# Optimization experiments

Hardware: AMD Instinct MI355X
Metric: run time of the kernel (lower is better)

The kernel has to match this reference:

```python
import jax, jax.numpy as jnp
import numpy as np

# Shapes / hyperparams (match init_kwargs and input_specs)
B, CIN, COUT, H, W = 8, 128, 128, 64, 64
K, S, P, D = 3, 1, 1, 1
KK = K * K
EPS = 1e-5  # BatchNorm eps


def setup_inputs() -> dict:
    key = jax.random.key(0)
    ks = jax.random.split(key, 4)
    x = jax.random.normal(ks[0], (B, CIN, H, W), jnp.float32)
    # small offset weights so predicted offsets stay O(1) pixels
    w_off = jax.random.normal(ks[1], (2 * KK, CIN, K, K), jnp.float32) * 0.01
    w_def = jax.random.normal(ks[2], (COUT, CIN, K, K), jnp.float32) * (1.0 / np.sqrt(CIN * KK))
    b_def = jax.random.normal(ks[3], (COUT,), jnp.float32) * 0.01
    gamma = jnp.ones((COUT,), jnp.float32)
    beta = jnp.zeros((COUT,), jnp.float32)
    return dict(x=x, w_off=w_off, w_def=w_def, b_def=b_def, gamma=gamma, beta=beta)


def _bilinear_gather(x, ys, xs):
    """x: [B,C,H,W]; ys/xs: [B,KK,Ho,Wo] float coords -> [B,C,KK,Ho,Wo].
    Zero padding outside the image (torchvision DeformConv2d semantics)."""
    Bb, C, Hh, Ww = x.shape
    y0 = jnp.floor(ys)
    x0 = jnp.floor(xs)
    wy = ys - y0
    wx = xs - x0
    xf = x.reshape(Bb, C, Hh * Ww)

    def gather(yi, xi, w):
        valid = (yi >= 0) & (yi < Hh) & (xi >= 0) & (xi < Ww)
        idx = (jnp.clip(yi, 0, Hh - 1) * Ww + jnp.clip(xi, 0, Ww - 1)).astype(jnp.int32)
        g = jnp.take_along_axis(xf, idx.reshape(Bb, 1, -1), axis=2)  # [B,C,KK*Ho*Wo]
        g = g.reshape(Bb, C, *idx.shape[1:])  # [B,C,KK,Ho,Wo]
        return g * (w * valid)[:, None]

    return (gather(y0, x0, (1 - wy) * (1 - wx))
            + gather(y0, x0 + 1, (1 - wy) * wx)
            + gather(y0 + 1, x0, wy * (1 - wx))
            + gather(y0 + 1, x0 + 1, wy * wx))


def _forward(x, w_off, w_def, b_def, gamma, beta):
    # 1) offset prediction: standard conv, no bias
    offset = jax.lax.conv_general_dilated(
        x, w_off, window_strides=(S, S), padding=((P, P), (P, P)),
        rhs_dilation=(D, D), dimension_numbers=('NCHW', 'OIHW', 'NCHW'))
    Ho, Wo = offset.shape[2], offset.shape[3]
    off = offset.reshape(B, KK, 2, Ho, Wo)  # (dy, dx) pairs per kernel loc
    dy, dx = off[:, :, 0], off[:, :, 1]

    # 2) deformable sampling coordinates
    ky = (jnp.arange(KK) // K).astype(jnp.float32) * D  # kernel row offset
    kx = (jnp.arange(KK) % K).astype(jnp.float32) * D   # kernel col offset
    base_y = (jnp.arange(Ho) * S - P).astype(jnp.float32)
    base_x = (jnp.arange(Wo) * S - P).astype(jnp.float32)
    ys = base_y[None, None, :, None] + ky[None, :, None, None] + dy  # [B,KK,Ho,Wo]
    xs = base_x[None, None, None, :] + kx[None, :, None, None] + dx

    sampled = _bilinear_gather(x, ys, xs)  # [B,CIN,KK,Ho,Wo]

    # 3) per-kernel-location weighted accumulation (implicit GEMM) + bias
    out = jnp.einsum('bckhw,ock->bohw', sampled, w_def.reshape(COUT, CIN, KK))
    out = out + b_def[None, :, None, None]

    # 4) BatchNorm2d (training mode: batch statistics) + SiLU
    mean = out.mean(axis=(0, 2, 3))
    var = out.var(axis=(0, 2, 3))
    scale = gamma / jnp.sqrt(var + EPS)
    out = (out - mean[None, :, None, None]) * scale[None, :, None, None] + beta[None, :, None, None]
    return out * jax.nn.sigmoid(out)  # SiLU


def reference(x, w_off, w_def, b_def, gamma, beta):
    return _forward(x, w_off, w_def, b_def, gamma, beta)
```

## Files before the change

### kernel.cpp

```cpp
#include <hip/hip_runtime.h>
#include <math.h>

#define CIN   128
#define COUT  128
#define KKT   9
#define NSTAT 32768.0f

typedef __attribute__((ext_vector_type(8))) short bf16x8;
typedef __attribute__((ext_vector_type(4))) float f32x4;
typedef __attribute__((ext_vector_type(2))) float f32x2;

__device__ inline unsigned short f2bf(float f) {
    union { float f; unsigned u; } v; v.f = f;
    unsigned r = v.u + 0x7fffu + ((v.u >> 16) & 1u);
    return (unsigned short)(r >> 16);
}
__device__ inline f32x2 bf2(unsigned u) {
    union { unsigned u; float f; } lo, hi;
    lo.u = u << 16; hi.u = u & 0xffff0000u;
    f32x2 r; r[0] = lo.f; r[1] = hi.f; return r;
}

#define PUB_BARRIER() do { asm volatile("s_waitcnt lgkmcnt(0)" ::: "memory"); \
                           __builtin_amdgcn_s_barrier(); } while (0)


__global__ __launch_bounds__(512) void prep_all_k(const float* __restrict__ x,
                                                  unsigned* __restrict__ xt,
                                                  const float* __restrict__ w_def,
                                                  const float* __restrict__ w_off,
                                                  unsigned short* __restrict__ wb,
                                                  unsigned short* __restrict__ wob,
                                                  float* __restrict__ sums) {
    __shared__ float lt[128][65];
    const int bb = blockIdx.x;
    if (bb < 512) {
        const int b = bb >> 6, y = bb & 63;
        const int t = threadIdx.x, l = t & 63, g8 = t >> 6;
        const float* xb = x + (b * 128) * 4096 + y * 64;
#pragma unroll
        for (int pass = 0; pass < 16; pass++) {
            int c = pass * 8 + g8;
            lt[c][l] = xb[c * 4096 + l];
        }
        __syncthreads();
        unsigned* xo = xt + (bb * 64) * 64;
#pragma unroll
        for (int pass = 0; pass < 8; pass++) {
            int w = pass * 8 + g8;
            float f0 = lt[2 * l][w], f1 = lt[2 * l + 1][w];
            xo[w * 64 + l] = (unsigned)f2bf(f0) | ((unsigned)f2bf(f1) << 16);
        }
    } else {
        int i = (bb - 512) * 512 + threadIdx.x;
        if (i < 147456) {
            int oc = i / 1152, r = i - oc * 1152, kt = r >> 7, c = r & 127;
            wb[i] = f2bf(w_def[(oc * 128 + c) * 9 + kt]);
        } else if (i < 147456 + 36864) {
            int j = i - 147456;
            int ocp = j / 1152, r = j - ocp * 1152, kt = r >> 7, c = r & 127;
            wob[j] = (ocp < 18) ? f2bf(w_off[(ocp * 128 + c) * 9 + kt]) : (unsigned short)0;
        } else if (i < 147456 + 36864 + 256) {
            sums[i - 147456 - 36864] = 0.f;
        }
    }
}

__global__ __launch_bounds__(1024, 8) void deform_main_k(const unsigned* __restrict__ xt,
                                                         const unsigned short* __restrict__ wb,
                                                         const unsigned short* __restrict__ wob,
                                                         const float* __restrict__ b_def,
                                                         float* __restrict__ out,
                                                         float* __restrict__ sums,
                                                         float* __restrict__ sumsq) {
    __shared__ __align__(16) unsigned char smem[52224];
    unsigned short* xrow  = (unsigned short*)smem;
    int*            tab   = (int*)smem;
    unsigned short* samp0 = (unsigned short*)(smem + 18432);
    unsigned short* samp1 = (unsigned short*)(smem + 34816);
    float* offl = (float*)(smem + 34816);
    float* stat = (float*)(smem + 51200);

    const int t    = threadIdx.x;
    const int bh   = blockIdx.x;
    const int b    = bh >> 6;
    const int j_   = bh & 63;
    const int h    = ((j_ & 7) << 3) | (j_ >> 3);
    const int lane = t & 63;
    const int wv   = __builtin_amdgcn_readfirstlane(t >> 6);
    const int quad = lane >> 4, lo = lane & 15;
    const int l    = lane;
    const int g    = lane >> 2;

    const unsigned* xtb = xt + b * 262144;

#pragma unroll
    for (int it = 0; it < 13; it++) {
        int p = wv + it * 16;
        if (p < 198) {
            int r = p / 66, xi = p - r * 66;
            int y = h + r - 1, x = xi - 1;
            unsigned u = 0;
            if ((unsigned)y < 64u && (unsigned)x < 64u) u = xtb[(y * 64 + x) * 64 + l];
            ((unsigned*)xrow)[(r * 66 + xi) * 64 + ((g ^ (xi & 15)) << 2) + (l & 3)] = u;
        }
    }
    __syncthreads();

    const int omt = wv >> 2, ont = wv & 3;
    f32x4 ao = {0.f, 0.f, 0.f, 0.f};
    if (wv < 8) {
        const unsigned short* wrow = wob + (omt * 16 + lo) * 1152 + quad * 8;
        for (int kt = 0; kt < 9; kt++) {
            int ky = kt / 3, kx = kt - ky * 3;
            int xi = ont * 16 + lo + kx;
#pragma unroll
            for (int ch = 0; ch < 4; ch++) {
                int gg = ch * 4 + quad;
                bf16x8 af = *(const bf16x8*)(wrow + kt * 128 + ch * 32);
                bf16x8 bf = *(const bf16x8*)(xrow + (ky * 66 + xi) * 128 + ((gg ^ (xi & 15)) << 3));
                ao = __builtin_amdgcn_mfma_f32_16x16x32_bf16(af, bf, ao, 0, 0, 0);
            }
        }
    }
    __syncthreads();
    if (wv < 8) {
#pragma unroll
        for (int r = 0; r < 4; r++) {
            int oc = omt * 16 + quad * 4 + r;
            if (oc < 18) offl[oc * 64 + ont * 16 + lo] = ao[r];
        }
    }
    __syncthreads();

    for (int i = t; i < KKT * 64; i += 1024) {
        int k = i >> 6, w2 = i & 63;
        float dy = offl[(2 * k) * 64 + w2];
        float dx = offl[(2 * k + 1) * 64 + w2];
        int ky = k / 3, kx = k - ky * 3;
        float ys = (float)(h - 1 + ky) + dy;
        float xs = (float)(w2 - 1 + kx) + dx;
        float y0f = floorf(ys), x0f = floorf(xs);
        float wyf = ys - y0f, wxf = xs - x0f;
        int iy0 = (int)y0f, ix0 = (int)x0f;
        int cy0 = min(max(iy0, 0), 63), cy1 = min(max(iy0 + 1, 0), 63);
        int px  = min(max(ix0, 0), 63), px2 = min(max(ix0 + 1, 0), 63);
        float wy0 = (iy0 >= 0 && iy0 < 64) ? (1.f - wyf) : 0.f;
        float wy1 = (iy0 + 1 >= 0 && iy0 + 1 < 64) ? wyf : 0.f;
        float wa  = (ix0 >= 0 && ix0 < 64) ? (1.f - wxf) : 0.f;
        float wbv = (ix0 + 1 >= 0 && ix0 + 1 < 64) ? wxf : 0.f;
        int base = i * 8;
        tab[base + 0] = (cy0 * 64 + px ) * 64;
        tab[base + 1] = (cy0 * 64 + px2) * 64;
        tab[base + 2] = (cy1 * 64 + px ) * 64;
        tab[base + 3] = (cy1 * 64 + px2) * 64;
        ((float*)tab)[base + 4] = wy0 * wa;
        ((float*)tab)[base + 5] = wy0 * wbv;
        ((float*)tab)[base + 6] = wy1 * wa;
        ((float*)tab)[base + 7] = wy1 * wbv;
    }
    if (t < 256) stat[t] = 0.f;
    __syncthreads();

    const int ot  = wv & 7;
    const int ph  = wv >> 3;
    const int w0p = wv * 4;
    f32x4 acc[2];
#pragma unroll
    for (int j = 0; j < 2; j++)
#pragma unroll
        for (int r = 0; r < 4; r++) acc[j][r] = 0.f;

    const unsigned short* wrow = wb + (ot * 16 + lo) * 1152 + quad * 8;

    unsigned u0[4], u1[4], u2[4], u3[4];
#pragma unroll
    for (int i = 0; i < 4; i++) {
        const int4 a = *(const int4*)&tab[(w0p + i) * 8];
        u0[i] = xtb[a.x + l]; u1[i] = xtb[a.y + l];
        u2[i] = xtb[a.z + l]; u3[i] = xtb[a.w + l];
    }

    for (int kt = 0; kt < KKT; kt++) {
        unsigned* sb = (unsigned*)((kt & 1) ? samp1 : samp0);
#pragma unroll
        for (int i = 0; i < 4; i++) {
            const float4 tw = *(const float4*)&tab[(kt * 64 + w0p + i) * 8 + 4];
            f32x2 s = bf2(u0[i]) * tw.x;
            s += bf2(u1[i]) * tw.y;
            s += bf2(u2[i]) * tw.z;
            s += bf2(u3[i]) * tw.w;
            unsigned pk;
            asm("v_cvt_pk_bf16_f32 %0, %1, %2" : "=v"(pk) : "v"(s[0]), "v"(s[1]));
            int w = w0p + i;
            sb[w * 64 + ((g ^ (w & 15)) << 2) + (l & 3)] = pk;
        }
        if (kt < KKT - 1) {
#pragma unroll
            for (int i = 0; i < 4; i++) {
                const int4 a = *(const int4*)&tab[((kt + 1) * 64 + w0p + i) * 8];
                u0[i] = xtb[a.x + l]; u1[i] = xtb[a.y + l];
                u2[i] = xtb[a.z + l]; u3[i] = xtb[a.w + l];
            }
        }
        PUB_BARRIER();
        const unsigned short* sbs = (kt & 1) ? samp1 : samp0;
#pragma unroll
        for (int ch = 0; ch < 4; ch++) {
            bf16x8 af = *(const bf16x8*)(wrow + kt * 128 + ch * 32);
            int gg = ch * 4 + quad;
#pragma unroll
            for (int jj = 0; jj < 2; jj++) {
                int j = 2 * ph + jj;
                bf16x8 bfv = *(const bf16x8*)(sbs + (j * 16 + lo) * 128 + ((gg ^ lo) << 3));
                acc[jj] = __builtin_amdgcn_mfma_f32_16x16x32_bf16(af, bfv, acc[jj], 0, 0, 0);
            }
        }
    }

    float* ob = out + b * COUT * 4096 + h * 64;
#pragma unroll
    for (int r = 0; r < 4; r++) {
        int oc = ot * 16 + quad * 4 + r;
        float bia = b_def[oc];
        float ssum = 0.f, qsum = 0.f;
#pragma unroll
        for (int jj = 0; jj < 2; jj++) {
            int j = 2 * ph + jj;
            float v = acc[jj][r] + bia;
            ob[oc * 4096 + j * 16 + lo] = v;
            ssum += v; qsum += v * v;
        }
#pragma unroll
        for (int d = 1; d < 16; d <<= 1) {
            ssum += __shfl_xor(ssum, d, 64);
            qsum += __shfl_xor(qsum, d, 64);
        }
        if (lo == 0) { atomicAdd(&stat[oc], ssum); atomicAdd(&stat[128 + oc], qsum); }
    }
    __syncthreads();
    if (t < 256) {
        float* gp = (t < 128) ? (sums + t) : (sumsq + (t - 128));
        atomicAdd(gp, stat[t]);
    }
}

__global__ __launch_bounds__(256) void bn_silu_k(float* __restrict__ out,
                                                 const float* __restrict__ sums,
                                                 const float* __restrict__ sumsq,
                                                 const float* __restrict__ gamma,
                                                 const float* __restrict__ beta) {
    __shared__ float sc_s[128], sh_s[128];
    int t = threadIdx.x;
    if (t < 128) {
        const float invN = 1.f / NSTAT;
        float m = sums[t] * invN;
        float v = fmaf(-m, m, sumsq[t] * invN);
        float sc = gamma[t] * rsqrtf(v + 1e-5f);
        sc_s[t] = sc;
        sh_s[t] = beta[t] - m * sc;
    }
    __syncthreads();
    int i = blockIdx.x * 256 + t;
    float4 v = ((float4*)out)[i];
    int oc = (i >> 10) & 127;
    float sc = sc_s[oc], sh = sh_s[oc];
    float z0 = v.x * sc + sh;
    float z1 = v.y * sc + sh;
    float z2 = v.z * sc + sh;
    float z3 = v.w * sc + sh;
    v.x = z0 / (1.f + __expf(-z0));
    v.y = z1 / (1.f + __expf(-z1));
    v.z = z2 / (1.f + __expf(-z2));
    v.w = z3 / (1.f + __expf(-z3));
    ((float4*)out)[i] = v;
}

extern "C" void kernel_launch(void* const* d_in, const int* in_sizes, int n_in,
                              void* d_out, int out_size, void* d_ws, size_t ws_size,
                              hipStream_t stream) {
    const float* x     = (const float*)d_in[0];
    const float* w_off = (const float*)d_in[1];
    const float* w_def = (const float*)d_in[2];
    const float* b_def = (const float*)d_in[3];
    const float* gamma = (const float*)d_in[4];
    const float* beta  = (const float*)d_in[5];
    float* out = (float*)d_out;

    unsigned*       xt   = (unsigned*)d_ws;
    unsigned short* wb   = (unsigned short*)((char*)d_ws + 16777216);
    unsigned short* wob  = (unsigned short*)((char*)d_ws + 17072128);
    float*          sums = (float*)((char*)d_ws + 17145856);
    float*          sumsq = sums + 128;

    prep_all_k<<<873, 512, 0, stream>>>(x, xt, w_def, w_off, wb, wob, sums);
    deform_main_k<<<512, 1024, 0, stream>>>(xt, wb, wob, b_def, out, sums, sumsq);
    bn_silu_k<<<4096, 256, 0, stream>>>(out, sums, sumsq, gamma, beta);
}
```

Baseline: 153.6 us.

## Build bilinear samples directly in MFMA B registers, dropping LDS sample staging

The main loop now has each lane gather four 16-byte neighbour vectors from global memory and blend them straight into the MFMA B operand. This removes the double-buffered LDS sample tile and the per-tap barrier. Blocks shrink to 512 threads, and each wave computes four 16-channel output tiles that share the one blended B fragment. The gain is no LDS round trip or sync per tap, paid for with more A-weight loads per wave, more gathers in flight and higher register pressure.

Result: slower. 235.7 us (+53.5%).

```diff
diff --git a/kernel.cpp b/kernel.cpp
--- a/kernel.cpp
+++ b/kernel.cpp
@@ -20,9 +20,16 @@
     lo.u = u << 16; hi.u = u & 0xffff0000u;
     f32x2 r; r[0] = lo.f; r[1] = hi.f; return r;
 }
-
-#define PUB_BARRIER() do { asm volatile("s_waitcnt lgkmcnt(0)" ::: "memory"); \
-                           __builtin_amdgcn_s_barrier(); } while (0)
+__device__ inline unsigned blend1(unsigned c00, unsigned c01, unsigned c10, unsigned c11,
+                                  float w00, float w01, float w10, float w11) {
+    f32x2 s = bf2(c00) * w00;
+    s += bf2(c01) * w01;
+    s += bf2(c10) * w10;
+    s += bf2(c11) * w11;
+    unsigned pk;
+    asm("v_cvt_pk_bf16_f32 %0, %1, %2" : "=v"(pk) : "v"(s[0]), "v"(s[1]));
+    return pk;
+}
 
 
 __global__ __launch_bounds__(512) void prep_all_k(const float* __restrict__ x,
@@ -66,20 +73,18 @@
     }
 }
 
-__global__ __launch_bounds__(1024, 8) void deform_main_k(const unsigned* __restrict__ xt,
-                                                         const unsigned short* __restrict__ wb,
-                                                         const unsigned short* __restrict__ wob,
-                                                         const float* __restrict__ b_def,
-                                                         float* __restrict__ out,
-                                                         float* __restrict__ sums,
-                                                         float* __restrict__ sumsq) {
-    __shared__ __align__(16) unsigned char smem[52224];
-    unsigned short* xrow  = (unsigned short*)smem;
-    int*            tab   = (int*)smem;
-    unsigned short* samp0 = (unsigned short*)(smem + 18432);
-    unsigned short* samp1 = (unsigned short*)(smem + 34816);
-    float* offl = (float*)(smem + 34816);
-    float* stat = (float*)(smem + 51200);
+__global__ __launch_bounds__(512, 4) void deform_main_k(const unsigned* __restrict__ xt,
+                                                        const unsigned short* __restrict__ wb,
+                                                        const unsigned short* __restrict__ wob,
+                                                        const float* __restrict__ b_def,
+                                                        float* __restrict__ out,
+                                                        float* __restrict__ sums,
+                                                        float* __restrict__ sumsq) {
+    __shared__ __align__(16) unsigned char smem[51712];
+    unsigned short* xrow = (unsigned short*)smem;
+    int*            tab  = (int*)smem;
+    float* offl = (float*)(smem + 18432);
+    float* stat = (float*)(smem + 50688);
 
     const int t    = threadIdx.x;
     const int bh   = blockIdx.x;
@@ -95,8 +100,8 @@
     const unsigned* xtb = xt + b * 262144;
 
 #pragma unroll
-    for (int it = 0; it < 13; it++) {
-        int p = wv + it * 16;
+    for (int it = 0; it < 25; it++) {
+        int p = wv + it * 8;
         if (p < 198) {
             int r = p / 66, xi = p - r * 66;
             int y = h + r - 1, x = xi - 1;
@@ -107,9 +112,9 @@
     }
     __syncthreads();
 
-    const int omt = wv >> 2, ont = wv & 3;
-    f32x4 ao = {0.f, 0.f, 0.f, 0.f};
-    if (wv < 8) {
+    {
+        const int omt = wv >> 2, ont = wv & 3;
+        f32x4 ao = {0.f, 0.f, 0.f, 0.f};
         const unsigned short* wrow = wob + (omt * 16 + lo) * 1152 + quad * 8;
         for (int kt = 0; kt < 9; kt++) {
             int ky = kt / 3, kx = kt - ky * 3;
@@ -122,9 +127,7 @@
                 ao = __builtin_amdgcn_mfma_f32_16x16x32_bf16(af, bf, ao, 0, 0, 0);
             }
         }
-    }
-    __syncthreads();
-    if (wv < 8) {
+        __syncthreads();
 #pragma unroll
         for (int r = 0; r < 4; r++) {
             int oc = omt * 16 + quad * 4 + r;
@@ -133,13 +136,13 @@
     }
     __syncthreads();
 
-    for (int i = t; i < KKT * 64; i += 1024) {
-        int k = i >> 6, w2 = i & 63;
-        float dy = offl[(2 * k) * 64 + w2];
-        float dx = offl[(2 * k + 1) * 64 + w2];
+    for (int i = t; i < KKT * 64; i += 512) {
+        int k = i >> 6, w2i = i & 63;
+        float dy = offl[(2 * k) * 64 + w2i];
+        float dx = offl[(2 * k + 1) * 64 + w2i];
         int ky = k / 3, kx = k - ky * 3;
         float ys = (float)(h - 1 + ky) + dy;
-        float xs = (float)(w2 - 1 + kx) + dx;
+        float xs = (float)(w2i - 1 + kx) + dx;
         float y0f = floorf(ys), x0f = floorf(xs);
         float wyf = ys - y0f, wxf = xs - x0f;
         int iy0 = (int)y0f, ix0 = (int)x0f;
@@ -150,10 +153,10 @@
         float wa  = (ix0 >= 0 && ix0 < 64) ? (1.f - wxf) : 0.f;
         float wbv = (ix0 + 1 >= 0 && ix0 + 1 < 64) ? wxf : 0.f;
         int base = i * 8;
-        tab[base + 0] = (cy0 * 64 + px ) * 64;
-        tab[base + 1] = (cy0 * 64 + px2) * 64;
-        tab[base + 2] = (cy1 * 64 + px ) * 64;
-        tab[base + 3] = (cy1 * 64 + px2) * 64;
+        tab[base + 0] = (cy0 * 64 + px ) * 16;
+        tab[base + 1] = (cy0 * 64 + px2) * 16;
+        tab[base + 2] = (cy1 * 64 + px ) * 16;
+        tab[base + 3] = (cy1 * 64 + px2) * 16;
         ((float*)tab)[base + 4] = wy0 * wa;
         ((float*)tab)[base + 5] = wy0 * wbv;
         ((float*)tab)[base + 6] = wy1 * wa;
@@ -162,81 +165,66 @@
     if (t < 256) stat[t] = 0.f;
     __syncthreads();
 
-    const int ot  = wv & 7;
-    const int ph  = wv >> 3;
-    const int w0p = wv * 4;
-    f32x4 acc[2];
-#pragma unroll
-    for (int j = 0; j < 2; j++)
-#pragma unroll
-        for (int r = 0; r < 4; r++) acc[j][r] = 0.f;
-
-    const unsigned short* wrow = wb + (ot * 16 + lo) * 1152 + quad * 8;
-
-    unsigned u0[4], u1[4], u2[4], u3[4];
-#pragma unroll
-    for (int i = 0; i < 4; i++) {
-        const int4 a = *(const int4*)&tab[(w0p + i) * 8];
-        u0[i] = xtb[a.x + l]; u1[i] = xtb[a.y + l];
-        u2[i] = xtb[a.z + l]; u3[i] = xtb[a.w + l];
-    }
+    const int nt = wv & 3, oh = wv >> 2;
+    const int w2 = nt * 16 + lo;
+    const uint4* xt4 = (const uint4*)xtb;
+    const unsigned short* abase = wb + (oh * 64 + lo) * 1152 + quad * 8;
+
+    f32x4 acc[4];
+#pragma unroll
+    for (int a = 0; a < 4; a++)
+#pragma unroll
+        for (int r = 0; r < 4; r++) acc[a][r] = 0.f;
+
+    int4   cb = *(const int4*)&tab[w2 * 8];
+    float4 tw = *(const float4*)&tab[w2 * 8 + 4];
 
     for (int kt = 0; kt < KKT; kt++) {
-        unsigned* sb = (unsigned*)((kt & 1) ? samp1 : samp0);
-#pragma unroll
-        for (int i = 0; i < 4; i++) {
-            const float4 tw = *(const float4*)&tab[(kt * 64 + w0p + i) * 8 + 4];
-            f32x2 s = bf2(u0[i]) * tw.x;
-            s += bf2(u1[i]) * tw.y;
-            s += bf2(u2[i]) * tw.z;
-            s += bf2(u3[i]) * tw.w;
-            unsigned pk;
-            asm("v_cvt_pk_bf16_f32 %0, %1, %2" : "=v"(pk) : "v"(s[0]), "v"(s[1]));
-            int w = w0p + i;
-            sb[w * 64 + ((g ^ (w & 15)) << 2) + (l & 3)] = pk;
-        }
-        if (kt < KKT - 1) {
-#pragma unroll
-            for (int i = 0; i < 4; i++) {
-                const int4 a = *(const int4*)&tab[((kt + 1) * 64 + w0p + i) * 8];
-                u0[i] = xtb[a.x + l]; u1[i] = xtb[a.y + l];
-                u2[i] = xtb[a.z + l]; u3[i] = xtb[a.w + l];
+        int ktn = (kt + 1 < KKT) ? kt + 1 : kt;
+        int4   cbn = *(const int4*)&tab[(ktn * 64 + w2) * 8];
+        float4 twn = *(const float4*)&tab[(ktn * 64 + w2) * 8 + 4];
+#pragma unroll
+        for (int ch = 0; ch < 4; ch++) {
+            const int co = ch * 4 + quad;
+            uint4 c00 = xt4[cb.x + co];
+            uint4 c01 = xt4[cb.y + co];
+            uint4 c10 = xt4[cb.z + co];
+            uint4 c11 = xt4[cb.w + co];
+            const unsigned short* ap = abase + kt * 128 + ch * 32;
+            bf16x8 a0 = *(const bf16x8*)(ap);
+            bf16x8 a1 = *(const bf16x8*)(ap + 18432);
+            bf16x8 a2 = *(const bf16x8*)(ap + 36864);
+            bf16x8 a3 = *(const bf16x8*)(ap + 55296);
+            uint4 bq;
+            bq.x = blend1(c00.x, c01.x, c10.x, c11.x, tw.x, tw.y, tw.z, tw.w);
+            bq.y = blend1(c00.y, c01.y, c10.y, c11.y, tw.x, tw.y, tw.z, tw.w);
+            bq.z = blend1(c00.z, c01.z, c10.z, c11.z, tw.x, tw.y, tw.z, tw.w);
+            bq.w = blend1(c00.w, c01.w, c10.w, c11.w, tw.x, tw.y, tw.z, tw.w);
+            bf16x8 bfv = *(bf16x8*)&bq;
+            acc[0] = __builtin_amdgcn_mfma_f32_16x16x32_bf16(a0, bfv, acc[0], 0, 0, 0);
+            acc[1] = __builtin_amdgcn_mfma_f32_16x16x32_bf16(a1, bfv, acc[1], 0, 0, 0);
+            acc[2] = __builtin_amdgcn_mfma_f32_16x16x32_bf16(a2, bfv, acc[2], 0, 0, 0);
+            acc[3] = __builtin_amdgcn_mfma_f32_16x16x32_bf16(a3, bfv, acc[3], 0, 0, 0);
+        }
+        cb = cbn; tw = twn;
+    }
+
+    float* ob = out + b * COUT * 4096 + h * 64;
+#pragma unroll
+    for (int a = 0; a < 4; a++) {
+#pragma unroll
+        for (int r = 0; r < 4; r++) {
+            int oc = (oh * 4 + a) * 16 + quad * 4 + r;
+            float v = acc[a][r] + b_def[oc];
+            ob[oc * 4096 + w2] = v;
+            float ssum = v, qsum = v * v;
+#pragma unroll
+            for (int d = 1; d < 16; d <<= 1) {
+                ssum += __shfl_xor(ssum, d, 64);
+                qsum += __shfl_xor(qsum, d, 64);
             }
-        }
-        PUB_BARRIER();
-        const unsigned short* sbs = (kt & 1) ? samp1 : samp0;
-#pragma unroll
-        for (int ch = 0; ch < 4; ch++) {
-            bf16x8 af = *(const bf16x8*)(wrow + kt * 128 + ch * 32);
-            int gg = ch * 4 + quad;
-#pragma unroll
-            for (int jj = 0; jj < 2; jj++) {
-                int j = 2 * ph + jj;
-                bf16x8 bfv = *(const bf16x8*)(sbs + (j * 16 + lo) * 128 + ((gg ^ lo) << 3));
-                acc[jj] = __builtin_amdgcn_mfma_f32_16x16x32_bf16(af, bfv, acc[jj], 0, 0, 0);
-            }
-        }
-    }
-
-    float* ob = out + b * COUT * 4096 + h * 64;
-#pragma unroll
-    for (int r = 0; r < 4; r++) {
-        int oc = ot * 16 + quad * 4 + r;
-        float bia = b_def[oc];
-        float ssum = 0.f, qsum = 0.f;
-#pragma unroll
-        for (int jj = 0; jj < 2; jj++) {
-            int j = 2 * ph + jj;
-            float v = acc[jj][r] + bia;
-            ob[oc * 4096 + j * 16 + lo] = v;
-            ssum += v; qsum += v * v;
-        }
-#pragma unroll
-        for (int d = 1; d < 16; d <<= 1) {
-            ssum += __shfl_xor(ssum, d, 64);
-            qsum += __shfl_xor(qsum, d, 64);
-        }
-        if (lo == 0) { atomicAdd(&stat[oc], ssum); atomicAdd(&stat[128 + oc], qsum); }
+            if (lo == 0) { atomicAdd(&stat[oc], ssum); atomicAdd(&stat[128 + oc], qsum); }
+        }
     }
     __syncthreads();
     if (t < 256) {
@@ -294,6 +282,6 @@
     float*          sumsq = sums + 128;
 
     prep_all_k<<<873, 512, 0, stream>>>(x, xt, w_def, w_off, wb, wob, sums);
-    deform_main_k<<<512, 1024, 0, stream>>>(xt, wb, wob, b_def, out, sums, sumsq);
+    deform_main_k<<<512, 512, 0, stream>>>(xt, wb, wob, b_def, out, sums, sumsq);
     bn_silu_k<<<4096, 256, 0, stream>>>(out, sums, sumsq, gamma, beta);
 }
```

## Split main loop into producer and consumer warps for gather and MFMA

Applied to the files above, without the earlier changes.

Warp-specialises the deformable main loop. Waves 0-7 only gather bilinear samples (8 columns each) into the double-buffered sample tile one kernel tap ahead. Waves 8-15 only run MFMAs, each covering all 64 columns for one 16-channel output tile, with the weight fragments for the next tap prefetched into registers. The offset buffer moves to its own LDS region, so shared memory grows. The aim is to overlap gather latency with matrix work, at the cost of half the waves holding more live registers and extra LDS.

Measured after the change: 197.3 us. 28.5% more time.

```diff
diff --git a/kernel.cpp b/kernel.cpp
--- a/kernel.cpp
+++ b/kernel.cpp
@@ -73,13 +73,13 @@
                                                          float* __restrict__ out,
                                                          float* __restrict__ sums,
                                                          float* __restrict__ sumsq) {
-    __shared__ __align__(16) unsigned char smem[52224];
+    __shared__ __align__(16) unsigned char smem[56832];
     unsigned short* xrow  = (unsigned short*)smem;
     int*            tab   = (int*)smem;
     unsigned short* samp0 = (unsigned short*)(smem + 18432);
     unsigned short* samp1 = (unsigned short*)(smem + 34816);
-    float* offl = (float*)(smem + 34816);
-    float* stat = (float*)(smem + 51200);
+    float* offl = (float*)(smem + 51200);
+    float* stat = (float*)(smem + 55808);
 
     const int t    = threadIdx.x;
     const int bh   = blockIdx.x;
@@ -92,6 +92,8 @@
     const int l    = lane;
     const int g    = lane >> 2;
 
+    if (t < 256) stat[t] = 0.f;
+
     const unsigned* xtb = xt + b * 262144;
 
 #pragma unroll
@@ -107,39 +109,41 @@
     }
     __syncthreads();
 
-    const int omt = wv >> 2, ont = wv & 3;
-    f32x4 ao = {0.f, 0.f, 0.f, 0.f};
-    if (wv < 8) {
-        const unsigned short* wrow = wob + (omt * 16 + lo) * 1152 + quad * 8;
-        for (int kt = 0; kt < 9; kt++) {
-            int ky = kt / 3, kx = kt - ky * 3;
-            int xi = ont * 16 + lo + kx;
-#pragma unroll
-            for (int ch = 0; ch < 4; ch++) {
-                int gg = ch * 4 + quad;
-                bf16x8 af = *(const bf16x8*)(wrow + kt * 128 + ch * 32);
-                bf16x8 bf = *(const bf16x8*)(xrow + (ky * 66 + xi) * 128 + ((gg ^ (xi & 15)) << 3));
-                ao = __builtin_amdgcn_mfma_f32_16x16x32_bf16(af, bf, ao, 0, 0, 0);
-            }
-        }
-    }
-    __syncthreads();
-    if (wv < 8) {
-#pragma unroll
-        for (int r = 0; r < 4; r++) {
-            int oc = omt * 16 + quad * 4 + r;
-            if (oc < 18) offl[oc * 64 + ont * 16 + lo] = ao[r];
+    {
+        const int omt = wv >> 2, ont = wv & 3;
+        f32x4 ao = {0.f, 0.f, 0.f, 0.f};
+        if (wv < 8) {
+            const unsigned short* wrow = wob + (omt * 16 + lo) * 1152 + quad * 8;
+            for (int kt = 0; kt < 9; kt++) {
+                int ky = kt / 3, kx = kt - ky * 3;
+                int xi = ont * 16 + lo + kx;
+#pragma unroll
+                for (int ch = 0; ch < 4; ch++) {
+                    int gg = ch * 4 + quad;
+                    bf16x8 af = *(const bf16x8*)(wrow + kt * 128 + ch * 32);
+                    bf16x8 bf = *(const bf16x8*)(xrow + (ky * 66 + xi) * 128 + ((gg ^ (xi & 15)) << 3));
+                    ao = __builtin_amdgcn_mfma_f32_16x16x32_bf16(af, bf, ao, 0, 0, 0);
+                }
+            }
+        }
+        __syncthreads();
+        if (wv < 8) {
+#pragma unroll
+            for (int r = 0; r < 4; r++) {
+                int oc = omt * 16 + quad * 4 + r;
+                if (oc < 18) offl[oc * 64 + ont * 16 + lo] = ao[r];
+            }
         }
     }
     __syncthreads();
 
     for (int i = t; i < KKT * 64; i += 1024) {
-        int k = i >> 6, w2 = i & 63;
-        float dy = offl[(2 * k) * 64 + w2];
-        float dx = offl[(2 * k + 1) * 64 + w2];
+        int k = i >> 6, w2i = i & 63;
+        float dy = offl[(2 * k) * 64 + w2i];
+        float dx = offl[(2 * k + 1) * 64 + w2i];
         int ky = k / 3, kx = k - ky * 3;
         float ys = (float)(h - 1 + ky) + dy;
-        float xs = (float)(w2 - 1 + kx) + dx;
+        float xs = (float)(w2i - 1 + kx) + dx;
         float y0f = floorf(ys), x0f = floorf(xs);
         float wyf = ys - y0f, wxf = xs - x0f;
         int iy0 = (int)y0f, ix0 = (int)x0f;
@@ -159,84 +163,99 @@
         ((float*)tab)[base + 6] = wy1 * wa;
         ((float*)tab)[base + 7] = wy1 * wbv;
     }
-    if (t < 256) stat[t] = 0.f;
-    __syncthreads();
-
-    const int ot  = wv & 7;
-    const int ph  = wv >> 3;
-    const int w0p = wv * 4;
-    f32x4 acc[2];
-#pragma unroll
-    for (int j = 0; j < 2; j++)
-#pragma unroll
-        for (int r = 0; r < 4; r++) acc[j][r] = 0.f;
-
-    const unsigned short* wrow = wb + (ot * 16 + lo) * 1152 + quad * 8;
-
-    unsigned u0[4], u1[4], u2[4], u3[4];
-#pragma unroll
-    for (int i = 0; i < 4; i++) {
-        const int4 a = *(const int4*)&tab[(w0p + i) * 8];
-        u0[i] = xtb[a.x + l]; u1[i] = xtb[a.y + l];
-        u2[i] = xtb[a.z + l]; u3[i] = xtb[a.w + l];
-    }
-
-    for (int kt = 0; kt < KKT; kt++) {
-        unsigned* sb = (unsigned*)((kt & 1) ? samp1 : samp0);
-#pragma unroll
-        for (int i = 0; i < 4; i++) {
-            const float4 tw = *(const float4*)&tab[(kt * 64 + w0p + i) * 8 + 4];
+    __syncthreads();
+
+    const bool prod = (wv < 8);
+    const int  ot   = wv - 8;
+    const int  w0p  = wv << 3;
+
+    unsigned u0[8], u1[8], u2[8], u3[8];
+    f32x4 acc[4];
+    bf16x8 afc[4];
+    const unsigned short* abase = wb + ((ot < 0 ? 0 : ot) * 16 + lo) * 1152 + quad * 8;
+
+#pragma unroll
+    for (int n = 0; n < 4; n++)
+#pragma unroll
+        for (int r = 0; r < 4; r++) acc[n][r] = 0.f;
+
+    auto produce = [&](int k) {
+#pragma unroll
+        for (int i = 0; i < 8; i++) {
+            int w = w0p + i;
+            const int4 a = *(const int4*)&tab[(k * 64 + w) * 8];
+            u0[i] = xtb[a.x + l]; u1[i] = xtb[a.y + l];
+            u2[i] = xtb[a.z + l]; u3[i] = xtb[a.w + l];
+        }
+        unsigned* sb = (unsigned*)((k & 1) ? samp1 : samp0);
+#pragma unroll
+        for (int i = 0; i < 8; i++) {
+            int w = w0p + i;
+            const float4 tw = *(const float4*)&tab[(k * 64 + w) * 8 + 4];
             f32x2 s = bf2(u0[i]) * tw.x;
             s += bf2(u1[i]) * tw.y;
             s += bf2(u2[i]) * tw.z;
             s += bf2(u3[i]) * tw.w;
             unsigned pk;
             asm("v_cvt_pk_bf16_f32 %0, %1, %2" : "=v"(pk) : "v"(s[0]), "v"(s[1]));
-            int w = w0p + i;
             sb[w * 64 + ((g ^ (w & 15)) << 2) + (l & 3)] = pk;
         }
-        if (kt < KKT - 1) {
-#pragma unroll
-            for (int i = 0; i < 4; i++) {
-                const int4 a = *(const int4*)&tab[((kt + 1) * 64 + w0p + i) * 8];
-                u0[i] = xtb[a.x + l]; u1[i] = xtb[a.y + l];
-                u2[i] = xtb[a.z + l]; u3[i] = xtb[a.w + l];
-            }
+    };
+
+    if (prod) {
+        produce(0);
+    } else {
+#pragma unroll
+        for (int ch = 0; ch < 4; ch++)
+            afc[ch] = *(const bf16x8*)(abase + ch * 32);
+    }
+    PUB_BARRIER();
+
+    for (int kt = 0; kt < KKT; kt++) {
+        if (prod) {
+            if (kt < KKT - 1) produce(kt + 1);
+        } else {
+            int ktn = (kt < KKT - 1) ? kt + 1 : kt;
+            bf16x8 afn[4];
+#pragma unroll
+            for (int ch = 0; ch < 4; ch++)
+                afn[ch] = *(const bf16x8*)(abase + ktn * 128 + ch * 32);
+            const unsigned short* sbs = (kt & 1) ? samp1 : samp0;
+#pragma unroll
+            for (int ch = 0; ch < 4; ch++) {
+                int gg = ch * 4 + quad;
+#pragma unroll
+                for (int n = 0; n < 4; n++) {
+                    bf16x8 bfv = *(const bf16x8*)(sbs + (n * 16 + lo) * 128 + ((gg ^ lo) << 3));
+                    acc[n] = __builtin_amdgcn_mfma_f32_16x16x32_bf16(afc[ch], bfv, acc[n], 0, 0, 0);
+                }
+            }
+#pragma unroll
+            for (int ch = 0; ch < 4; ch++) afc[ch] = afn[ch];
         }
         PUB_BARRIER();
-        const unsigned short* sbs = (kt & 1) ? samp1 : samp0;
-#pragma unroll
-        for (int ch = 0; ch < 4; ch++) {
-            bf16x8 af = *(const bf16x8*)(wrow + kt * 128 + ch * 32);
-            int gg = ch * 4 + quad;
-#pragma unroll
-            for (int jj = 0; jj < 2; jj++) {
-                int j = 2 * ph + jj;
-                bf16x8 bfv = *(const bf16x8*)(sbs + (j * 16 + lo) * 128 + ((gg ^ lo) << 3));
-                acc[jj] = __builtin_amdgcn_mfma_f32_16x16x32_bf16(af, bfv, acc[jj], 0, 0, 0);
-            }
-        }
-    }
-
-    float* ob = out + b * COUT * 4096 + h * 64;
-#pragma unroll
-    for (int r = 0; r < 4; r++) {
-        int oc = ot * 16 + quad * 4 + r;
-        float bia = b_def[oc];
-        float ssum = 0.f, qsum = 0.f;
-#pragma unroll
-        for (int jj = 0; jj < 2; jj++) {
-            int j = 2 * ph + jj;
-            float v = acc[jj][r] + bia;
-            ob[oc * 4096 + j * 16 + lo] = v;
-            ssum += v; qsum += v * v;
-        }
-#pragma unroll
-        for (int d = 1; d < 16; d <<= 1) {
-            ssum += __shfl_xor(ssum, d, 64);
-            qsum += __shfl_xor(qsum, d, 64);
-        }
-        if (lo == 0) { atomicAdd(&stat[oc], ssum); atomicAdd(&stat[128 + oc], qsum); }
+    }
+
+    if (!prod) {
+        float* ob = out + b * COUT * 4096 + h * 64;
+#pragma unroll
+        for (int r = 0; r < 4; r++) {
+            int oc = ot * 16 + quad * 4 + r;
+            float bia = b_def[oc];
+            float ssum = 0.f, qsum = 0.f;
+#pragma unroll
+            for (int n = 0; n < 4; n++) {
+                float v = acc[n][r] + bia;
+                ob[oc * 4096 + n * 16 + lo] = v;
+                ssum += v; qsum += v * v;
+            }
+#pragma unroll
+            for (int d = 1; d < 16; d <<= 1) {
+                ssum += __shfl_xor(ssum, d, 64);
+                qsum += __shfl_xor(qsum, d, 64);
+            }
+            if (lo == 0) { atomicAdd(&stat[oc], ssum); atomicAdd(&stat[128 + oc], qsum); }
+        }
     }
     __syncthreads();
     if (t < 256) {
```

## Split fused deform kernel into offset-table and gather-GEMM kernels with half-row blocks

Applied to the files above, without the earlier changes.

The single 1024-thread kernel that computed offsets, the bilinear table and the GEMM is split in two. The first kernel computes offsets and writes a compact sampling table (packed 16-bit addresses plus weights) to global memory. The second launches twice as many 512-thread blocks, each handling half a row, with less shared memory so more blocks fit per CU. The aim is better occupancy and less idle time for the waves that sat out the offset phase. The cost is an extra launch, a global round trip for the table, and per-wave global atomics in place of a block-level reduction for the statistics.

Result: slower. 236.6 us (+54.0%).

```diff
diff --git a/kernel.cpp b/kernel.cpp
--- a/kernel.cpp
+++ b/kernel.cpp
@@ -66,20 +66,12 @@
     }
 }
 
-__global__ __launch_bounds__(1024, 8) void deform_main_k(const unsigned* __restrict__ xt,
-                                                         const unsigned short* __restrict__ wb,
-                                                         const unsigned short* __restrict__ wob,
-                                                         const float* __restrict__ b_def,
-                                                         float* __restrict__ out,
-                                                         float* __restrict__ sums,
-                                                         float* __restrict__ sumsq) {
-    __shared__ __align__(16) unsigned char smem[52224];
-    unsigned short* xrow  = (unsigned short*)smem;
-    int*            tab   = (int*)smem;
-    unsigned short* samp0 = (unsigned short*)(smem + 18432);
-    unsigned short* samp1 = (unsigned short*)(smem + 34816);
-    float* offl = (float*)(smem + 34816);
-    float* stat = (float*)(smem + 51200);
+__global__ __launch_bounds__(512, 4) void offset_tab_k(const unsigned* __restrict__ xt,
+                                                       const unsigned short* __restrict__ wob,
+                                                       int* __restrict__ tabg) {
+    __shared__ __align__(16) unsigned char smem[55296];
+    unsigned short* xrow = (unsigned short*)smem;
+    float* offl = (float*)(smem + 50688);
 
     const int t    = threadIdx.x;
     const int bh   = blockIdx.x;
@@ -95,8 +87,8 @@
     const unsigned* xtb = xt + b * 262144;
 
 #pragma unroll
-    for (int it = 0; it < 13; it++) {
-        int p = wv + it * 16;
+    for (int it = 0; it < 25; it++) {
+        int p = wv + it * 8;
         if (p < 198) {
             int r = p / 66, xi = p - r * 66;
             int y = h + r - 1, x = xi - 1;
@@ -107,9 +99,9 @@
     }
     __syncthreads();
 
-    const int omt = wv >> 2, ont = wv & 3;
-    f32x4 ao = {0.f, 0.f, 0.f, 0.f};
-    if (wv < 8) {
+    {
+        const int omt = wv >> 2, ont = wv & 3;
+        f32x4 ao = {0.f, 0.f, 0.f, 0.f};
         const unsigned short* wrow = wob + (omt * 16 + lo) * 1152 + quad * 8;
         for (int kt = 0; kt < 9; kt++) {
             int ky = kt / 3, kx = kt - ky * 3;
@@ -122,9 +114,6 @@
                 ao = __builtin_amdgcn_mfma_f32_16x16x32_bf16(af, bf, ao, 0, 0, 0);
             }
         }
-    }
-    __syncthreads();
-    if (wv < 8) {
 #pragma unroll
         for (int r = 0; r < 4; r++) {
             int oc = omt * 16 + quad * 4 + r;
@@ -133,13 +122,14 @@
     }
     __syncthreads();
 
-    for (int i = t; i < KKT * 64; i += 1024) {
-        int k = i >> 6, w2 = i & 63;
-        float dy = offl[(2 * k) * 64 + w2];
-        float dx = offl[(2 * k + 1) * 64 + w2];
+    int* tb = tabg + bh * 3456;
+    for (int i = t; i < KKT * 64; i += 512) {
+        int k = i >> 6, w2i = i & 63;
+        float dy = offl[(2 * k) * 64 + w2i];
+        float dx = offl[(2 * k + 1) * 64 + w2i];
         int ky = k / 3, kx = k - ky * 3;
         float ys = (float)(h - 1 + ky) + dy;
-        float xs = (float)(w2 - 1 + kx) + dx;
+        float xs = (float)(w2i - 1 + kx) + dx;
         float y0f = floorf(ys), x0f = floorf(xs);
         float wyf = ys - y0f, wxf = xs - x0f;
         int iy0 = (int)y0f, ix0 = (int)x0f;
@@ -149,86 +139,121 @@
         float wy1 = (iy0 + 1 >= 0 && iy0 + 1 < 64) ? wyf : 0.f;
         float wa  = (ix0 >= 0 && ix0 < 64) ? (1.f - wxf) : 0.f;
         float wbv = (ix0 + 1 >= 0 && ix0 + 1 < 64) ? wxf : 0.f;
-        int base = i * 8;
-        tab[base + 0] = (cy0 * 64 + px ) * 64;
-        tab[base + 1] = (cy0 * 64 + px2) * 64;
-        tab[base + 2] = (cy1 * 64 + px ) * 64;
-        tab[base + 3] = (cy1 * 64 + px2) * 64;
-        ((float*)tab)[base + 4] = wy0 * wa;
-        ((float*)tab)[base + 5] = wy0 * wbv;
-        ((float*)tab)[base + 6] = wy1 * wa;
-        ((float*)tab)[base + 7] = wy1 * wbv;
-    }
-    if (t < 256) stat[t] = 0.f;
+        int a0 = cy0 * 64 + px, a1 = cy0 * 64 + px2;
+        int a2 = cy1 * 64 + px, a3 = cy1 * 64 + px2;
+        int base = k * 384 + w2i * 6;
+        int2 ap; ap.x = a0 | (a1 << 16); ap.y = a2 | (a3 << 16);
+        *(int2*)(tb + base) = ap;
+        float2 wA; wA.x = wy0 * wa; wA.y = wy0 * wbv;
+        float2 wB; wB.x = wy1 * wa; wB.y = wy1 * wbv;
+        *(float2*)(tb + base + 2) = wA;
+        *(float2*)(tb + base + 4) = wB;
+    }
+}
+
+__global__ __launch_bounds__(512, 4) void deform_gemm_k(const unsigned* __restrict__ xt,
+                                                        const int* __restrict__ tabg,
+                                                        const unsigned short* __restrict__ wb,
+                                                        const float* __restrict__ b_def,
+                                                        float* __restrict__ out,
+                                                        float* __restrict__ sums,
+                                                        float* __restrict__ sumsq) {
+    __shared__ __align__(16) unsigned char smem[23296];
+    int*            tabl  = (int*)smem;
+    unsigned short* samp0 = (unsigned short*)(smem + 6912);
+    unsigned short* samp1 = (unsigned short*)(smem + 15104);
+
+    const int t    = threadIdx.x;
+    const int bid  = blockIdx.x;
+    const int bh   = bid & 511;
+    const int half = bid >> 9;
+    const int b    = bh >> 6;
+    const int j_   = bh & 63;
+    const int h    = ((j_ & 7) << 3) | (j_ >> 3);
+    const int lane = t & 63;
+    const int wv   = __builtin_amdgcn_readfirstlane(t >> 6);
+    const int quad = lane >> 4, lo = lane & 15;
+    const int l    = lane;
+    const int g    = lane >> 2;
+
+    const unsigned* xtb = xt + b * 262144;
+
+    const int* tg = tabg + bh * 3456 + half * 192;
+    for (int i = t; i < 1728; i += 512) {
+        int kt = i / 192, j = i - kt * 192;
+        tabl[kt * 192 + j] = tg[kt * 384 + j];
+    }
     __syncthreads();
 
-    const int ot  = wv & 7;
-    const int ph  = wv >> 3;
-    const int w0p = wv * 4;
+    const int p0 = wv * 4;
     f32x4 acc[2];
 #pragma unroll
-    for (int j = 0; j < 2; j++)
-#pragma unroll
-        for (int r = 0; r < 4; r++) acc[j][r] = 0.f;
-
-    const unsigned short* wrow = wb + (ot * 16 + lo) * 1152 + quad * 8;
-
+    for (int n = 0; n < 2; n++)
+#pragma unroll
+        for (int r = 0; r < 4; r++) acc[n][r] = 0.f;
+
+    const unsigned short* abase = wb + (wv * 16 + lo) * 1152 + quad * 8;
     unsigned u0[4], u1[4], u2[4], u3[4];
-#pragma unroll
-    for (int i = 0; i < 4; i++) {
-        const int4 a = *(const int4*)&tab[(w0p + i) * 8];
-        u0[i] = xtb[a.x + l]; u1[i] = xtb[a.y + l];
-        u2[i] = xtb[a.z + l]; u3[i] = xtb[a.w + l];
-    }
+
+#define GATHER(k_)                                                        \
+    do {                                                                  \
+        _Pragma("unroll")                                                 \
+        for (int i = 0; i < 4; i++) {                                     \
+            int p = p0 + i;                                               \
+            int2 ap = *(const int2*)&tabl[(k_) * 192 + p * 6];            \
+            unsigned a0 = (unsigned)ap.x & 0xffffu, a1 = (unsigned)ap.x >> 16; \
+            unsigned a2 = (unsigned)ap.y & 0xffffu, a3 = (unsigned)ap.y >> 16; \
+            u0[i] = xtb[(a0 << 6) + l]; u1[i] = xtb[(a1 << 6) + l];       \
+            u2[i] = xtb[(a2 << 6) + l]; u3[i] = xtb[(a3 << 6) + l];       \
+        }                                                                 \
+    } while (0)
+
+    GATHER(0);
 
     for (int kt = 0; kt < KKT; kt++) {
         unsigned* sb = (unsigned*)((kt & 1) ? samp1 : samp0);
 #pragma unroll
         for (int i = 0; i < 4; i++) {
-            const float4 tw = *(const float4*)&tab[(kt * 64 + w0p + i) * 8 + 4];
-            f32x2 s = bf2(u0[i]) * tw.x;
-            s += bf2(u1[i]) * tw.y;
-            s += bf2(u2[i]) * tw.z;
-            s += bf2(u3[i]) * tw.w;
+            int p = p0 + i;
+            float2 wA = *(const float2*)&tabl[kt * 192 + p * 6 + 2];
+            float2 wB = *(const float2*)&tabl[kt * 192 + p * 6 + 4];
+            f32x2 s = bf2(u0[i]) * wA.x;
+            s += bf2(u1[i]) * wA.y;
+            s += bf2(u2[i]) * wB.x;
+            s += bf2(u3[i]) * wB.y;
             unsigned pk;
             asm("v_cvt_pk_bf16_f32 %0, %1, %2" : "=v"(pk) : "v"(s[0]), "v"(s[1]));
-            int w = w0p + i;
-            sb[w * 64 + ((g ^ (w & 15)) << 2) + (l & 3)] = pk;
-        }
-        if (kt < KKT - 1) {
-#pragma unroll
-            for (int i = 0; i < 4; i++) {
-                const int4 a = *(const int4*)&tab[((kt + 1) * 64 + w0p + i) * 8];
-                u0[i] = xtb[a.x + l]; u1[i] = xtb[a.y + l];
-                u2[i] = xtb[a.z + l]; u3[i] = xtb[a.w + l];
-            }
-        }
+            sb[p * 64 + ((g ^ (p & 15)) << 2) + (l & 3)] = pk;
+        }
+        if (kt < KKT - 1) GATHER(kt + 1);
         PUB_BARRIER();
         const unsigned short* sbs = (kt & 1) ? samp1 : samp0;
+        bf16x8 af[4];
+#pragma unroll
+        for (int ch = 0; ch < 4; ch++)
+            af[ch] = *(const bf16x8*)(abase + kt * 128 + ch * 32);
 #pragma unroll
         for (int ch = 0; ch < 4; ch++) {
-            bf16x8 af = *(const bf16x8*)(wrow + kt * 128 + ch * 32);
             int gg = ch * 4 + quad;
 #pragma unroll
-            for (int jj = 0; jj < 2; jj++) {
-                int j = 2 * ph + jj;
-                bf16x8 bfv = *(const bf16x8*)(sbs + (j * 16 + lo) * 128 + ((gg ^ lo) << 3));
-                acc[jj] = __builtin_amdgcn_mfma_f32_16x16x32_bf16(af, bfv, acc[jj], 0, 0, 0);
+            for (int n = 0; n < 2; n++) {
+                bf16x8 bfv = *(const bf16x8*)(sbs + (n * 16 + lo) * 128 + ((gg ^ lo) << 3));
+                acc[n] = __builtin_amdgcn_mfma_f32_16x16x32_bf16(af[ch], bfv, acc[n], 0, 0, 0);
             }
         }
     }
-
-    float* ob = out + b * COUT * 4096 + h * 64;
+#undef GATHER
+
+    float* ob = out + b * COUT * 4096 + h * 64 + half * 32;
 #pragma unroll
     for (int r = 0; r < 4; r++) {
-        int oc = ot * 16 + quad * 4 + r;
+        int oc = wv * 16 + quad * 4 + r;
         float bia = b_def[oc];
         float ssum = 0.f, qsum = 0.f;
 #pragma unroll
-        for (int jj = 0; jj < 2; jj++) {
-            int j = 2 * ph + jj;
-            float v = acc[jj][r] + bia;
-            ob[oc * 4096 + j * 16 + lo] = v;
+        for (int n = 0; n < 2; n++) {
+            float v = acc[n][r] + bia;
+            ob[oc * 4096 + n * 16 + lo] = v;
             ssum += v; qsum += v * v;
         }
 #pragma unroll
@@ -236,12 +261,10 @@
             ssum += __shfl_xor(ssum, d, 64);
             qsum += __shfl_xor(qsum, d, 64);
         }
-        if (lo == 0) { atomicAdd(&stat[oc], ssum); atomicAdd(&stat[128 + oc], qsum); }
-    }
-    __syncthreads();
-    if (t < 256) {
-        float* gp = (t < 128) ? (sums + t) : (sumsq + (t - 128));
-        atomicAdd(gp, stat[t]);
+        if (lo == 0) {
+            atomicAdd(&sums[oc], ssum);
+            atomicAdd(&sumsq[oc], qsum);
+        }
     }
 }
 
@@ -288,12 +311,14 @@
     float* out = (float*)d_out;
 
     unsigned*       xt   = (unsigned*)d_ws;
-    unsigned short* wb   = (unsigned short*)((char*)d_ws + 16777216);
-    unsigned short* wob  = (unsigned short*)((char*)d_ws + 17072128);
-    float*          sums = (float*)((char*)d_ws + 17145856);
+    int*            tabg = (int*)((char*)d_ws + 8388608);
+    unsigned short* wb   = (unsigned short*)((char*)d_ws + 15466496);
+    unsigned short* wob  = (unsigned short*)((char*)d_ws + 15761408);
+    float*          sums = (float*)((char*)d_ws + 15835136);
     float*          sumsq = sums + 128;
 
     prep_all_k<<<873, 512, 0, stream>>>(x, xt, w_def, w_off, wb, wob, sums);
-    deform_main_k<<<512, 1024, 0, stream>>>(xt, wb, wob, b_def, out, sums, sumsq);
+    offset_tab_k<<<512, 512, 0, stream>>>(xt, wob, tabg);
+    deform_gemm_k<<<1024, 512, 0, stream>>>(xt, tabg, wb, b_def, out, sums, sumsq);
     bn_silu_k<<<4096, 256, 0, stream>>>(out, sums, sumsq, gamma, beta);
 }
```
